# Optimization experiments

Measured on AMD Instinct MI355X. Metric: run time of the kernel, lower is better.

## Reference

```python
import jax, jax.numpy as jnp
import numpy as np

IN_DIM = 3072
OUT_DIM = 3072
NUM_GROUPS = 12
RANK = 1024
IN_PG = IN_DIM // NUM_GROUPS    # 256
OUT_PG = OUT_DIM // NUM_GROUPS  # 256


def _xavier_uniform(key, shape):
    # torch xavier_uniform on a 3D tensor treats dim0*..*dim[-2] as fan_in-ish;
    # torch uses fan_in = shape[-1]*prod(shape[1:-1])? Actually for >2D,
    # fan_in = shape[1] * receptive_field, fan_out = shape[0] * receptive_field.
    # For (g, i, r): fan_in = i * r? torch: fan_in = size(1)*rf, fan_out = size(0)*rf
    # where rf = prod(shape[2:]). So fan_in = shape[1]*shape[2], fan_out = shape[0]*shape[2].
    rf = int(np.prod(shape[2:])) if len(shape) > 2 else 1
    fan_in = shape[1] * rf
    fan_out = shape[0] * rf
    limit = float(np.sqrt(6.0 / (fan_in + fan_out)))
    return jax.random.uniform(key, shape, jnp.float32, -limit, limit)


def setup_inputs() -> dict:
    key = jax.random.key(0)
    kx, kd, ku = jax.random.split(key, 3)
    x = jax.random.normal(kx, (2, 4096, IN_DIM), jnp.float32)
    down = _xavier_uniform(kd, (NUM_GROUPS, IN_PG, RANK))
    up = _xavier_uniform(ku, (NUM_GROUPS, RANK, OUT_PG))
    mix = jnp.zeros((NUM_GROUPS, NUM_GROUPS, RANK), jnp.float32)
    idx = jnp.arange(NUM_GROUPS)
    mix = mix.at[idx, idx, :].set(1.0)
    return {"x": x, "down": down, "mix": mix, "up": up}


def reference(x, down, mix, up):
    b, l, _ = x.shape
    xg = x.reshape(b, l, NUM_GROUPS, IN_PG)          # [b,l,g,i]
    z = jnp.einsum('blgi,gir->blgr', xg, down)       # grouped down-project
    z = jnp.einsum('blgr,ghr->blhr', z, mix)         # per-rank group mix (12x12)
    y = jnp.einsum('blhr,hro->blho', z, up)          # grouped up-project
    return y.reshape(b, l, OUT_DIM)
```

## Files before the change

kernel.cpp:

```cpp
#include <hip/hip_runtime.h>
#include <stdint.h>

typedef short  s16x8 __attribute__((ext_vector_type(8)));
typedef short  s16x4 __attribute__((ext_vector_type(4)));
typedef float  f32x4 __attribute__((ext_vector_type(4)));
typedef unsigned short ushort_t;

#define G_AS __attribute__((address_space(1)))
#define L_AS __attribute__((address_space(3)))

__device__ __forceinline__ void gl_lds16(const void* g, void* l) {
    __builtin_amdgcn_global_load_lds((const G_AS uint32_t*)g, (L_AS uint32_t*)l, 16, 0, 0);
}

__device__ __forceinline__ float b2f(ushort_t u) {
    union { uint32_t i; float f; } v; v.i = ((uint32_t)u) << 16; return v.f;
}
__device__ __forceinline__ ushort_t f2b(float f) {
    uint32_t x = __float_as_uint(f);
    x += 0x7FFF + ((x >> 16) & 1);
    return (ushort_t)(x >> 16);
}

#define MFMA16(a, b, c) __builtin_amdgcn_mfma_f32_16x16x32_bf16((a), (b), (c), 0, 0, 0)

__global__ __launch_bounds__(256) void k_cvt(const float* __restrict__ src,
                                             ushort_t* __restrict__ dst, int n8) {
    int idx = blockIdx.x * 256 + threadIdx.x;
    int stride = gridDim.x * 256;
    for (int i = idx; i < n8; i += stride) {
        f32x4 a = *(const f32x4*)(src + (size_t)i * 8);
        f32x4 b = *(const f32x4*)(src + (size_t)i * 8 + 4);
        s16x8 v;
#pragma unroll
        for (int j = 0; j < 4; ++j) { v[j] = (short)f2b(a[j]); v[j + 4] = (short)f2b(b[j]); }
        *(s16x8*)(dst + (size_t)i * 8) = v;
    }
}

__global__ __launch_bounds__(256) void k_transpose_up(const float* __restrict__ up,
                                                      ushort_t* __restrict__ upT) {
    int bid = blockIdx.x;
    int h  = bid >> 6;
    int rt = (bid >> 2) & 15;
    int ot = bid & 3;
    int r0 = rt << 6, o0 = ot << 6;
    __shared__ ushort_t tile[64][72];
    int t = threadIdx.x;
    const float* src = up + ((size_t)h << 18) + (size_t)r0 * 256 + o0;
#pragma unroll
    for (int p = 0; p < 2; ++p) {
        int rr = (t >> 3) + (p << 5);
        int cc = (t & 7) << 3;
        f32x4 va = *(const f32x4*)(src + rr * 256 + cc);
        f32x4 vb = *(const f32x4*)(src + rr * 256 + cc + 4);
#pragma unroll
        for (int j = 0; j < 4; ++j) {
            tile[rr][cc + j]     = f2b(va[j]);
            tile[rr][cc + 4 + j] = f2b(vb[j]);
        }
    }
    __syncthreads();
    ushort_t* dst = upT + ((size_t)h << 18) + (size_t)o0 * 1024 + r0;
#pragma unroll
    for (int p = 0; p < 2; ++p) {
        int oo = (t >> 3) + (p << 5);
        int rr = (t & 7) << 3;
        s16x8 v;
#pragma unroll
        for (int j = 0; j < 8; ++j) v[j] = (short)tile[rr + j][oo];
        *(s16x8*)(dst + (size_t)oo * 1024 + rr) = v;
    }
}

__global__ __launch_bounds__(256) void k_build_w(const ushort_t* __restrict__ downB,
                                                 const float* __restrict__ mixp,
                                                 const ushort_t* __restrict__ upT,
                                                 ushort_t* __restrict__ WT) {
    int bid = blockIdx.x;
    int gh = bid >> 2;
    int g = gh / 12, h = gh % 12;
    int it = (bid >> 1) & 1, ot = bid & 1;
    int i0 = it << 7, o0 = ot << 7;

    const ushort_t* A    = downB + ((size_t)g << 18);
    const ushort_t* Bt   = upT   + ((size_t)h << 18);
    const float*    mrow = mixp  + (size_t)(g * 12 + h) * 1024;

    __shared__ ushort_t As[128 * 64];
    __shared__ ushort_t Bs[128 * 64];

    int tid  = threadIdx.x;
    int lane = tid & 63, wave = tid >> 6;
    int wr = wave >> 1, wc = wave & 1;
    int lr = lane & 15;
    int kq = (lane >> 4) << 3;

    f32x4 acc[4][4] = {};

    for (int kk = 0; kk < 1024; kk += 64) {
        __syncthreads();
#pragma unroll
        for (int j = 0; j < 4; ++j) {
            int off = (j << 12) + (wave << 10) + (lane << 4);
            int row = off >> 7;
            int kc  = (off & 127) >> 1;
            gl_lds16(A  + (size_t)(i0 + row) * 1024 + kk + kc, (char*)As + off);
            gl_lds16(Bt + (size_t)(o0 + row) * 1024 + kk + kc, (char*)Bs + off);
        }
        __syncthreads();
#pragma unroll
        for (int ks = 0; ks < 64; ks += 32) {
            f32x4 m0 = *(const f32x4*)(mrow + kk + ks + kq);
            f32x4 m1 = *(const f32x4*)(mrow + kk + ks + kq + 4);
            float mf[8];
#pragma unroll
            for (int j = 0; j < 4; ++j) { mf[j] = m0[j]; mf[j + 4] = m1[j]; }

            s16x8 bfr[4];
#pragma unroll
            for (int b = 0; b < 4; ++b) {
                s16x8 raw = *(const s16x8*)&Bs[(wc * 64 + b * 16 + lr) * 64 + ks + kq];
#pragma unroll
                for (int j = 0; j < 8; ++j)
                    bfr[b][j] = (short)f2b(b2f((ushort_t)raw[j]) * mf[j]);
            }
            s16x8 afr[4];
#pragma unroll
            for (int a = 0; a < 4; ++a)
                afr[a] = *(const s16x8*)&As[(wr * 64 + a * 16 + lr) * 64 + ks + kq];
#pragma unroll
            for (int a = 0; a < 4; ++a)
#pragma unroll
                for (int b = 0; b < 4; ++b)
                    acc[a][b] = MFMA16(afr[a], bfr[b], acc[a][b]);
        }
    }

    int colbase = g * 256 + i0 + wr * 64;
    int rowbase = h * 256 + o0 + wc * 64;
#pragma unroll
    for (int a = 0; a < 4; ++a)
#pragma unroll
        for (int b = 0; b < 4; ++b) {
            int o = rowbase + b * 16 + lr;
            int i = colbase + a * 16 + ((lane >> 4) << 2);
            s16x4 pv;
#pragma unroll
            for (int v = 0; v < 4; ++v) pv[v] = (short)f2b(acc[a][b][v]);
            *(s16x4*)(WT + (size_t)o * 3072 + i) = pv;
        }
}

__global__ __launch_bounds__(256) void k_main(const ushort_t* __restrict__ X,
                                              const ushort_t* __restrict__ WT,
                                              float* __restrict__ Y) {
    int bid = blockIdx.x;
    int nt = bid % 24, tt = bid / 24;
    int t0 = tt << 7, n0 = nt << 7;

    __shared__ ushort_t As[128 * 64];
    __shared__ ushort_t Bs[128 * 64];

    int tid  = threadIdx.x;
    int lane = tid & 63, wave = tid >> 6;
    int wr = wave >> 1, wc = wave & 1;
    int lr = lane & 15;
    int kq = (lane >> 4) << 3;

    f32x4 acc[4][4] = {};

    for (int kk = 0; kk < 3072; kk += 64) {
        __syncthreads();
#pragma unroll
        for (int j = 0; j < 4; ++j) {
            int off = (j << 12) + (wave << 10) + (lane << 4);
            int row = off >> 7;
            int kc  = (off & 127) >> 1;
            gl_lds16(X  + (size_t)(t0 + row) * 3072 + kk + kc, (char*)As + off);
            gl_lds16(WT + (size_t)(n0 + row) * 3072 + kk + kc, (char*)Bs + off);
        }
        __syncthreads();
#pragma unroll
        for (int ks = 0; ks < 64; ks += 32) {
            s16x8 afr[4], bfr[4];
#pragma unroll
            for (int a = 0; a < 4; ++a)
                afr[a] = *(const s16x8*)&As[(wr * 64 + a * 16 + lr) * 64 + ks + kq];
#pragma unroll
            for (int b = 0; b < 4; ++b)
                bfr[b] = *(const s16x8*)&Bs[(wc * 64 + b * 16 + lr) * 64 + ks + kq];
#pragma unroll
            for (int a = 0; a < 4; ++a)
#pragma unroll
                for (int b = 0; b < 4; ++b)
                    acc[a][b] = MFMA16(afr[a], bfr[b], acc[a][b]);
        }
    }

    int trow = t0 + wr * 64;
    int ncol = n0 + wc * 64;
#pragma unroll
    for (int a = 0; a < 4; ++a)
#pragma unroll
        for (int b = 0; b < 4; ++b) {
            int n  = ncol + b * 16 + lr;
            int tr = trow + a * 16 + ((lane >> 4) << 2);
#pragma unroll
            for (int v = 0; v < 4; ++v)
                Y[(size_t)(tr + v) * 3072 + n] = acc[a][b][v];
        }
}

extern "C" void kernel_launch(void* const* d_in, const int* in_sizes, int n_in,
                              void* d_out, int out_size, void* d_ws, size_t ws_size,
                              hipStream_t stream) {
    const float* x    = (const float*)d_in[0];
    const float* down = (const float*)d_in[1];
    const float* mixp = (const float*)d_in[2];
    const float* up   = (const float*)d_in[3];
    float* out = (float*)d_out;

    ushort_t* WT    = (ushort_t*)d_ws;
    ushort_t* upT   = WT    + (size_t)3072 * 3072;
    ushort_t* downB = upT   + (size_t)12 * 256 * 1024;
    ushort_t* xB    = downB + (size_t)12 * 256 * 1024;

    k_cvt         <<<dim3(1536), dim3(256), 0, stream>>>(down, downB, 393216);
    k_transpose_up<<<dim3(768),  dim3(256), 0, stream>>>(up, upT);
    k_build_w     <<<dim3(576),  dim3(256), 0, stream>>>(downB, mixp, upT, WT);
    k_cvt         <<<dim3(2048), dim3(256), 0, stream>>>(x, xB, 3145728);
    k_main        <<<dim3(1536), dim3(256), 0, stream>>>(xB, WT, out);
}
```

Baseline: 454.8 us.

## Rewrite main GEMM as 256x256 tile, 8-wave, double-buffered pipelined kernel

Replaces the 128x128 single-buffered main GEMM with a 256x256-tile kernel using 8 waves, 128KB of dynamic LDS and double buffering. Global-to-LDS loads for the next k-step are issued in phases interleaved with MFMA work under explicit vmcnt waits and barriers. The LDS layout is XOR-swizzled to avoid bank conflicts, and blocks are remapped so consecutive blocks spread across XCDs. This is meant to hide memory latency and raise arithmetic intensity, at the cost of one block per CU and a fragile hand-written wait/barrier schedule.

```diff
diff --git a/kernel.cpp b/kernel.cpp
--- a/kernel.cpp
+++ b/kernel.cpp
@@ -152,63 +152,92 @@
         }
 }
 
-__global__ __launch_bounds__(256) void k_main(const ushort_t* __restrict__ X,
-                                              const ushort_t* __restrict__ WT,
-                                              float* __restrict__ Y) {
+#define BAR() __builtin_amdgcn_s_barrier()
+#define WAITV(n) asm volatile("s_waitcnt vmcnt(" #n ")" ::: "memory")
+#define WAITL() asm volatile("s_waitcnt lgkmcnt(0)" ::: "memory")
+
+__global__ __launch_bounds__(512, 1) void k_main8(const ushort_t* __restrict__ X,
+                                                  const ushort_t* __restrict__ WT,
+                                                  float* __restrict__ Y) {
+    extern __shared__ ushort_t lds[];
     int bid = blockIdx.x;
-    int nt = bid % 24, tt = bid / 24;
-    int t0 = tt << 7, n0 = nt << 7;
-
-    __shared__ ushort_t As[128 * 64];
-    __shared__ ushort_t Bs[128 * 64];
+    int wg  = (bid & 7) * 48 + (bid >> 3);
+    int tt = wg / 12, nt = wg % 12;
+    int m0 = tt << 8, n0 = nt << 8;
 
     int tid  = threadIdx.x;
-    int lane = tid & 63, wave = tid >> 6;
-    int wr = wave >> 1, wc = wave & 1;
+    int lane = tid & 63;
+    int wave = tid >> 6;
+    int wr = wave >> 2;
+    int wc = wave & 3;
     int lr = lane & 15;
-    int kq = (lane >> 4) << 3;
-
-    f32x4 acc[4][4] = {};
-
-    for (int kk = 0; kk < 3072; kk += 64) {
-        __syncthreads();
-#pragma unroll
-        for (int j = 0; j < 4; ++j) {
-            int off = (j << 12) + (wave << 10) + (lane << 4);
-            int row = off >> 7;
-            int kc  = (off & 127) >> 1;
-            gl_lds16(X  + (size_t)(t0 + row) * 3072 + kk + kc, (char*)As + off);
-            gl_lds16(WT + (size_t)(n0 + row) * 3072 + kk + kc, (char*)Bs + off);
-        }
-        __syncthreads();
-#pragma unroll
-        for (int ks = 0; ks < 64; ks += 32) {
-            s16x8 afr[4], bfr[4];
-#pragma unroll
-            for (int a = 0; a < 4; ++a)
-                afr[a] = *(const s16x8*)&As[(wr * 64 + a * 16 + lr) * 64 + ks + kq];
-#pragma unroll
-            for (int b = 0; b < 4; ++b)
-                bfr[b] = *(const s16x8*)&Bs[(wc * 64 + b * 16 + lr) * 64 + ks + kq];
-#pragma unroll
-            for (int a = 0; a < 4; ++a)
-#pragma unroll
-                for (int b = 0; b < 4; ++b)
-                    acc[a][b] = MFMA16(afr[a], bfr[b], acc[a][b]);
-        }
-    }
-
-    int trow = t0 + wr * 64;
-    int ncol = n0 + wc * 64;
-#pragma unroll
-    for (int a = 0; a < 4; ++a)
-#pragma unroll
-        for (int b = 0; b < 4; ++b) {
-            int n  = ncol + b * 16 + lr;
-            int tr = trow + a * 16 + ((lane >> 4) << 2);
+    int cq = lane >> 4;
+
+    auto STAGE = [&](int buf, int op, int kh, int t) {
+        const ushort_t* src = op ? WT : X;
+        int rb = op ? n0 : m0;
+        int kb = t * 64 + kh * 32;
+        ushort_t* base = lds + buf * 32768 + op * 16384 + kh * 8192;
+#pragma unroll
+        for (int j = 0; j < 2; ++j) {
+            int boff = (j << 13) + (tid << 4);
+            int r  = boff >> 6;
+            int ch = (boff >> 4) & 3;
+            int ks = kb + ((ch ^ ((r >> 1) & 3)) << 3);
+            gl_lds16(src + (size_t)(rb + r) * 3072 + ks, (char*)base + boff);
+        }
+    };
+    auto RD = [&](int buf, int op, int kh, int fr) -> s16x8 {
+        int row = (op ? wc * 64 : wr * 128) + fr * 16 + lr;
+        int off = buf * 32768 + op * 16384 + kh * 8192 + row * 32
+                + ((cq ^ ((row >> 1) & 3)) << 3);
+        return *(const s16x8*)(lds + off);
+    };
+
+    f32x4 acc[8][4] = {};
+    s16x8 af[4], bf[4];
+
+#define PH_READ_AB(mlo, kh) { _Pragma("unroll") for (int i = 0; i < 4; ++i) af[i] = RD(cur, 0, kh, (mlo) + i); \
+                              _Pragma("unroll") for (int i = 0; i < 4; ++i) bf[i] = RD(cur, 1, kh, i); }
+#define PH_READ_A(mlo, kh)  { _Pragma("unroll") for (int i = 0; i < 4; ++i) af[i] = RD(cur, 0, kh, (mlo) + i); }
+#define PH_MFMA(mlo)        { __builtin_amdgcn_s_setprio(1); \
+                              _Pragma("unroll") for (int mi = 0; mi < 4; ++mi) \
+                              _Pragma("unroll") for (int ni = 0; ni < 4; ++ni) \
+                                  acc[(mlo) + mi][ni] = MFMA16(af[mi], bf[ni], acc[(mlo) + mi][ni]); \
+                              __builtin_amdgcn_s_setprio(0); }
+
+    STAGE(0, 0, 0, 0); STAGE(0, 1, 0, 0); STAGE(0, 0, 1, 0); STAGE(0, 1, 1, 0);
+    WAITV(4); BAR();
+
+    int cur = 0;
+    for (int t = 0; t < 47; ++t) {
+        int nx = cur ^ 1;
+        PH_READ_AB(0, 0); STAGE(nx, 0, 0, t + 1);
+        BAR(); WAITL(); PH_MFMA(0); BAR();
+        PH_READ_A(4, 0);  STAGE(nx, 1, 0, t + 1);
+        BAR(); WAITL(); PH_MFMA(4); WAITV(4); BAR();
+        PH_READ_AB(0, 1); STAGE(nx, 0, 1, t + 1);
+        BAR(); WAITL(); PH_MFMA(0); BAR();
+        PH_READ_A(4, 1);  STAGE(nx, 1, 1, t + 1);
+        BAR(); WAITL(); PH_MFMA(4); WAITV(4); BAR();
+        cur = nx;
+    }
+    PH_READ_AB(0, 0); BAR(); WAITL(); PH_MFMA(0); BAR();
+    PH_READ_A(4, 0);  BAR(); WAITL(); PH_MFMA(4); WAITV(0); BAR();
+    PH_READ_AB(0, 1); BAR(); WAITL(); PH_MFMA(0); BAR();
+    PH_READ_A(4, 1);  BAR(); WAITL(); PH_MFMA(4);
+
+    int trow = m0 + wr * 128 + (cq << 2);
+    int ncol = n0 + wc * 64 + lr;
+#pragma unroll
+    for (int mi = 0; mi < 8; ++mi)
+#pragma unroll
+        for (int ni = 0; ni < 4; ++ni) {
+            int rr = trow + mi * 16;
+            int cc = ncol + ni * 16;
 #pragma unroll
             for (int v = 0; v < 4; ++v)
-                Y[(size_t)(tr + v) * 3072 + n] = acc[a][b][v];
+                Y[(size_t)(rr + v) * 3072 + cc] = acc[mi][ni][v];
         }
 }
 
@@ -226,9 +255,16 @@
     ushort_t* downB = upT   + (size_t)12 * 256 * 1024;
     ushort_t* xB    = downB + (size_t)12 * 256 * 1024;
 
+    static int lds_attr_set = 0;
+    if (!lds_attr_set) {
+        hipFuncSetAttribute((const void*)k_main8,
+                            hipFuncAttributeMaxDynamicSharedMemorySize, 131072);
+        lds_attr_set = 1;
+    }
+
     k_cvt         <<<dim3(1536), dim3(256), 0, stream>>>(down, downB, 393216);
     k_transpose_up<<<dim3(768),  dim3(256), 0, stream>>>(up, upT);
     k_build_w     <<<dim3(576),  dim3(256), 0, stream>>>(downB, mixp, upT, WT);
     k_cvt         <<<dim3(2048), dim3(256), 0, stream>>>(x, xB, 3145728);
-    k_main        <<<dim3(1536), dim3(256), 0, stream>>>(xB, WT, out);
-}
+    k_main8       <<<dim3(384),  dim3(512), 131072, stream>>>(xB, WT, out);
+}
```

Result: faster. 410.6 us (-9.7%).
